# Kernel tuning notes

Hardware: AMD Instinct MI355X
Metric: run time of the kernel (lower is better)

Reference implementation:

```python
import jax, jax.numpy as jnp
import numpy as np

N_NODES = 50000
N_EDGES = 1000000
NEG_SLOPE = 0.2


def _gat_layer(x, W, attn_l, attn_r, bias, src, dst, n_nodes):
    """DGL-style GATConv. x:[N,Fin], W:[H*D,Fin], attn_l/attn_r:[H,D], bias:[H*D].
    Returns [N, H*D] after ReLU activation (flattened heads)."""
    H, D = attn_l.shape
    h = (x @ W.T).reshape(n_nodes, H, D)                    # [N,H,D]
    el = jnp.sum(h * attn_l[None], axis=-1)                 # [N,H]
    er = jnp.sum(h * attn_r[None], axis=-1)                 # [N,H]
    e = jax.nn.leaky_relu(el[src] + er[dst], NEG_SLOPE)     # [E,H]
    # edge softmax over incoming edges per destination node
    emax = jax.ops.segment_max(e, dst, num_segments=n_nodes)  # [N,H]
    emax = jnp.where(jnp.isfinite(emax), emax, 0.0)
    a = jnp.exp(e - emax[dst])                               # [E,H]
    denom = jax.ops.segment_sum(a, dst, num_segments=n_nodes)  # [N,H]
    alpha = a / denom[dst]                                   # [E,H]
    msg = alpha[:, :, None] * h[src]                         # [E,H,D]
    out = jax.ops.segment_sum(msg, dst, num_segments=n_nodes)  # [N,H,D]
    out = out + bias.reshape(1, H, D)
    out = jax.nn.relu(out)
    return out.reshape(n_nodes, H * D)


def setup_inputs() -> dict:
    key = jax.random.key(0)
    ks = jax.random.split(key, 16)
    features = jax.random.normal(ks[0], (N_NODES, 25), dtype=jnp.float32)
    src = jax.random.randint(ks[1], (N_EDGES,), 0, N_NODES, dtype=jnp.int32)
    dst = jax.random.randint(ks[2], (N_EDGES,), 0, N_NODES, dtype=jnp.int32)

    def glorot(k, shape, fan):
        return jax.random.normal(k, shape, dtype=jnp.float32) * (1.0 / np.sqrt(fan))

    # layer 1: in=25, out=10, heads=4
    W1 = glorot(ks[3], (40, 25), 25)
    al1 = glorot(ks[4], (4, 10), 10)
    ar1 = glorot(ks[5], (4, 10), 10)
    b1 = jnp.zeros((40,), dtype=jnp.float32)
    # layer 2: in=40, out=25, heads=4
    W2 = glorot(ks[6], (100, 40), 40)
    al2 = glorot(ks[7], (4, 25), 25)
    ar2 = glorot(ks[8], (4, 25), 25)
    b2 = jnp.zeros((100,), dtype=jnp.float32)
    # layer 3: in=100, out=50, heads=1
    W3 = glorot(ks[9], (50, 100), 100)
    al3 = glorot(ks[10], (1, 50), 50)
    ar3 = glorot(ks[11], (1, 50), 50)
    b3 = jnp.zeros((50,), dtype=jnp.float32)
    # final fc: 50 -> 93
    fc_w = glorot(ks[12], (93, 50), 50)
    fc_b = jnp.zeros((93,), dtype=jnp.float32)
    return {
        "features": features, "src": src, "dst": dst,
        "W1": W1, "al1": al1, "ar1": ar1, "b1": b1,
        "W2": W2, "al2": al2, "ar2": ar2, "b2": b2,
        "W3": W3, "al3": al3, "ar3": ar3, "b3": b3,
        "fc_w": fc_w, "fc_b": fc_b,
    }


def reference(features, src, dst,
              W1, al1, ar1, b1,
              W2, al2, ar2, b2,
              W3, al3, ar3, b3,
              fc_w, fc_b):
    n = features.shape[0]
    h = _gat_layer(features, W1, al1, ar1, b1, src, dst, n)   # [N,40]
    h = _gat_layer(h, W2, al2, ar2, b2, src, dst, n)          # [N,100]
    h = _gat_layer(h, W3, al3, ar3, b3, src, dst, n)          # [N,50]
    return h @ fc_w.T + fc_b                                  # [N,93]
```

## Files before the change

### kernel.cpp

```cpp
#include <hip/hip_runtime.h>
#include <hip/hip_bf16.h>

#ifndef NEG_SLOPE
#define NEG_SLOPE 0.2f
#endif

static inline int cdiv(long long a, long long b) { return (int)((a + b - 1) / b); }

__device__ __forceinline__ float lrelu(float v) { return v > 0.f ? v : NEG_SLOPE * v; }

template <int FIN, int FOUT>
__global__ void k_linear(const float* __restrict__ x, const float* __restrict__ W,
                         float* __restrict__ h, int n_nodes) {
    __shared__ float Ws[FIN * FOUT];
    for (int i = threadIdx.x; i < FIN * FOUT; i += blockDim.x) {
        int f = i / FIN, k = i % FIN;
        Ws[k * FOUT + f] = W[i];
    }
    __syncthreads();
    int idx = blockIdx.x * blockDim.x + threadIdx.x;
    int total = n_nodes * FOUT;
    if (idx >= total) return;
    int n = idx / FOUT, f = idx % FOUT;
    const float* __restrict__ xr = x + (long long)n * FIN;
    float acc = 0.f;
#pragma unroll
    for (int k = 0; k < FIN; ++k) acc += xr[k] * Ws[k * FOUT + f];
    h[idx] = acc;
}

template <int H, int D>
__global__ void k_scores(const float* __restrict__ h, const float* __restrict__ al,
                         const float* __restrict__ ar, float* __restrict__ el,
                         float* __restrict__ er, int n_nodes) {
    int idx = blockIdx.x * blockDim.x + threadIdx.x;
    if (idx >= n_nodes * H) return;
    int n = idx / H, hh = idx % H;
    const float* __restrict__ hr = h + (long long)n * (H * D) + hh * D;
    float sl = 0.f, sr = 0.f;
#pragma unroll
    for (int d0 = 0; d0 < D; ++d0) {
        float v = hr[d0];
        sl += v * al[hh * D + d0];
        sr += v * ar[hh * D + d0];
    }
    el[idx] = sl;
    er[idx] = sr;
}

__global__ void k_deg(const int* __restrict__ dst, int* __restrict__ deg, int n_edges) {
    int e = blockIdx.x * blockDim.x + threadIdx.x;
    if (e >= n_edges) return;
    atomicAdd(&deg[dst[e]], 1);
}

__global__ void k_scan_block(const int* __restrict__ deg, int* __restrict__ incl,
                             int* __restrict__ blocksum, int n) {
    __shared__ int tmp[256];
    int t = threadIdx.x;
    int i = blockIdx.x * 256 + t;
    int v = (i < n) ? deg[i] : 0;
    tmp[t] = v;
    __syncthreads();
    for (int off = 1; off < 256; off <<= 1) {
        int add = (t >= off) ? tmp[t - off] : 0;
        __syncthreads();
        tmp[t] += add;
        __syncthreads();
    }
    if (i < n) incl[i] = tmp[t];
    if (t == 255) blocksum[blockIdx.x] = tmp[t];
}

__global__ void k_scan_top(const int* __restrict__ blocksum, int* __restrict__ blockoff, int nb) {
    __shared__ int tmp[256];
    int t = threadIdx.x;
    int base = 0;
    for (int c = 0; c < nb; c += 256) {
        int i = c + t;
        int v = (i < nb) ? blocksum[i] : 0;
        tmp[t] = v;
        __syncthreads();
        for (int off = 1; off < 256; off <<= 1) {
            int add = (t >= off) ? tmp[t - off] : 0;
            __syncthreads();
            tmp[t] += add;
            __syncthreads();
        }
        if (i < nb) blockoff[i] = base + tmp[t] - v;
        base += tmp[255];
        __syncthreads();
    }
}

__global__ void k_scan_finalize(const int* __restrict__ incl, const int* __restrict__ deg,
                                const int* __restrict__ blockoff, int* __restrict__ rowptr,
                                int n, int n_edges) {
    int i = blockIdx.x * blockDim.x + threadIdx.x;
    if (i < n) rowptr[i] = incl[i] - deg[i] + blockoff[i / 256];
    if (i == 0) rowptr[n] = n_edges;
}

__global__ void k_fill(const int* __restrict__ src, const int* __restrict__ dst,
                       const int* __restrict__ rowptr, int* __restrict__ cursor,
                       int* __restrict__ csr_src, int n_edges) {
    int e = blockIdx.x * blockDim.x + threadIdx.x;
    if (e >= n_edges) return;
    int d = dst[e];
    int pos = atomicAdd(&cursor[d], 1);
    csr_src[rowptr[d] + pos] = src[e];
}

__global__ void k_sort_wave(const int* __restrict__ rowptr, int* __restrict__ csr_src,
                            int n_nodes) {
    int wid = (blockIdx.x * blockDim.x + threadIdx.x) >> 6;
    int lane = threadIdx.x & 63;
    if (wid >= n_nodes) return;
    int s0 = rowptr[wid], e0 = rowptr[wid + 1];
    int d = e0 - s0;
    if (d <= 1) return;
    if (d <= 64) {
        int v = (lane < d) ? csr_src[s0 + lane] : 0x7FFFFFFF;
        int rank = 0;
        for (int k = 0; k < d; ++k) {
            int vk = __shfl(v, k);
            rank += (vk < v || (vk == v && k < lane)) ? 1 : 0;
        }
        if (lane < d) csr_src[s0 + rank] = v;
    } else if (lane == 0) {
        for (int a = s0 + 1; a < e0; ++a) {
            int key = csr_src[a];
            int b = a - 1;
            while (b >= s0 && csr_src[b] > key) { csr_src[b + 1] = csr_src[b]; --b; }
            csr_src[b + 1] = key;
        }
    }
}

template <int FOUT, int H, int D, int EB>
__global__ void k_node_gather(const int* __restrict__ rowptr, const int* __restrict__ csr_src,
                              const float* __restrict__ el, const float* __restrict__ er,
                              const float* __restrict__ h, const float* __restrict__ bias,
                              float* __restrict__ xout, int n_nodes) {
    constexpr int NF = (FOUT + 63) / 64;
    int wid = (blockIdx.x * blockDim.x + threadIdx.x) >> 6;
    int lane = threadIdx.x & 63;
    if (wid >= n_nodes) return;
    int start = rowptr[wid], end = rowptr[wid + 1];

    const int eidx = lane / H;
    const int hh_c = lane % H;
    const float er_c = er[wid * H + hh_c];

    float acc[NF], den[NF];
    int f_i[NF], hh_i[NF];
#pragma unroll
    for (int r = 0; r < NF; ++r) {
        int f = lane + r * 64;
        f_i[r] = f;
        hh_i[r] = (f < FOUT) ? (f / D) : 0;
        acc[r] = 0.f;
        den[r] = 0.f;
    }

    if (start < end) {
        int j0 = start;
        int nb = end - j0;
        if (nb > EB) nb = EB;
        int jj = j0 + (eidx < nb ? eidx : 0);
        int s_c = csr_src[jj];
        float e_c = el[s_c * H + hh_c];

        while (true) {
            int j1 = j0 + nb;
            int nb_n = end - j1;
            if (nb_n > EB) nb_n = EB;
            int s_n = 0;
            float e_n = 0.f;
            if (nb_n > 0) {
                int jj2 = j1 + (eidx < nb_n ? eidx : 0);
                s_n = csr_src[jj2];
                e_n = el[s_n * H + hh_c];
            }
            float p_c = expf(lrelu(e_c + er_c));

            float hv[EB * NF];
#pragma unroll
            for (int e = 0; e < EB; ++e) {
                if (e < nb) {
                    int s = __shfl(s_c, e * H);
                    const float* __restrict__ hrow = h + (long long)s * FOUT;
#pragma unroll
                    for (int r = 0; r < NF; ++r)
                        if (f_i[r] < FOUT) hv[e * NF + r] = hrow[f_i[r]];
                }
            }
#pragma unroll
            for (int e = 0; e < EB; ++e) {
                if (e < nb) {
#pragma unroll
                    for (int r = 0; r < NF; ++r) {
                        float p = __shfl(p_c, e * H + hh_i[r]);
                        if (f_i[r] < FOUT) {
                            den[r] += p;
                            acc[r] += p * hv[e * NF + r];
                        }
                    }
                }
            }
            if (nb_n <= 0) break;
            j0 = j1;
            nb = nb_n;
            s_c = s_n;
            e_c = e_n;
        }
    }

#pragma unroll
    for (int r = 0; r < NF; ++r) {
        if (f_i[r] < FOUT) {
            float val;
            if (end > start) val = acc[r] / den[r] + bias[f_i[r]];
            else val = bias[f_i[r]];
            xout[(long long)wid * FOUT + f_i[r]] = val > 0.f ? val : 0.f;
        }
    }
}

template <int FIN, int FOUT>
__global__ void k_fc(const float* __restrict__ x, const float* __restrict__ W,
                     const float* __restrict__ b, float* __restrict__ out, int n_nodes) {
    __shared__ float Ws[FIN * FOUT];
    for (int i = threadIdx.x; i < FIN * FOUT; i += blockDim.x) {
        int f = i / FIN, k = i % FIN;
        Ws[k * FOUT + f] = W[i];
    }
    __syncthreads();
    int idx = blockIdx.x * blockDim.x + threadIdx.x;
    if (idx >= n_nodes * FOUT) return;
    int n = idx / FOUT, f = idx % FOUT;
    const float* __restrict__ xr = x + (long long)n * FIN;
    float acc = b[f];
#pragma unroll
    for (int k = 0; k < FIN; ++k) acc += xr[k] * Ws[k * FOUT + f];
    out[idx] = acc;
}

template <int FIN, int FOUT, int H, int D, int EB>
static void gat_layer(const float* x, const float* W, const float* al, const float* ar,
                      const float* bias, const int* rowptr, const int* csr_src,
                      int n_nodes, float* bufH, float* el, float* er, float* xnext,
                      hipStream_t stream) {
    int tNF = n_nodes * FOUT;
    k_linear<FIN, FOUT><<<cdiv(tNF, 256), 256, 0, stream>>>(x, W, bufH, n_nodes);
    k_scores<H, D><<<cdiv(n_nodes * H, 256), 256, 0, stream>>>(bufH, al, ar, el, er, n_nodes);
    k_node_gather<FOUT, H, D, EB><<<cdiv((long long)n_nodes * 64, 256), 256, 0, stream>>>(
        rowptr, csr_src, el, er, bufH, bias, xnext, n_nodes);
}

extern "C" void kernel_launch(void* const* d_in, const int* in_sizes, int n_in,
                              void* d_out, int out_size, void* d_ws, size_t ws_size,
                              hipStream_t stream) {
    const float* features = (const float*)d_in[0];
    const int* src = (const int*)d_in[1];
    const int* dst = (const int*)d_in[2];
    const float* W1 = (const float*)d_in[3];
    const float* al1 = (const float*)d_in[4];
    const float* ar1 = (const float*)d_in[5];
    const float* b1 = (const float*)d_in[6];
    const float* W2 = (const float*)d_in[7];
    const float* al2 = (const float*)d_in[8];
    const float* ar2 = (const float*)d_in[9];
    const float* b2 = (const float*)d_in[10];
    const float* W3 = (const float*)d_in[11];
    const float* al3 = (const float*)d_in[12];
    const float* ar3 = (const float*)d_in[13];
    const float* b3 = (const float*)d_in[14];
    const float* fc_w = (const float*)d_in[15];
    const float* fc_b = (const float*)d_in[16];

    const int n_nodes = in_sizes[0] / 25;
    const int n_edges = in_sizes[1];
    const int nblocks_nodes = cdiv(n_nodes, 256);

    char* ws = (char*)d_ws;
    size_t off = 0;
    auto alloc = [&](size_t bytes) {
        char* p = ws + off;
        off += (bytes + 255) & ~(size_t)255;
        return p;
    };
    float* bufA = (float*)alloc((size_t)n_nodes * 100 * sizeof(float));
    float* bufH = (float*)alloc((size_t)n_nodes * 100 * sizeof(float));
    float* el = (float*)alloc((size_t)n_nodes * 4 * sizeof(float));
    float* er = (float*)alloc((size_t)n_nodes * 4 * sizeof(float));
    int* deg = (int*)alloc((size_t)n_nodes * sizeof(int));
    int* incl = (int*)alloc((size_t)n_nodes * sizeof(int));
    int* blocksum = (int*)alloc((size_t)nblocks_nodes * sizeof(int));
    int* blockoff = (int*)alloc((size_t)nblocks_nodes * sizeof(int));
    int* rowptr = (int*)alloc((size_t)(n_nodes + 1) * sizeof(int));
    int* cursor = (int*)alloc((size_t)n_nodes * sizeof(int));
    int* csr_src = (int*)alloc((size_t)n_edges * sizeof(int));
    (void)ws_size;

    hipMemsetAsync(deg, 0, (size_t)n_nodes * sizeof(int), stream);
    hipMemsetAsync(cursor, 0, (size_t)n_nodes * sizeof(int), stream);
    k_deg<<<cdiv(n_edges, 256), 256, 0, stream>>>(dst, deg, n_edges);
    k_scan_block<<<nblocks_nodes, 256, 0, stream>>>(deg, incl, blocksum, n_nodes);
    k_scan_top<<<1, 256, 0, stream>>>(blocksum, blockoff, nblocks_nodes);
    k_scan_finalize<<<cdiv(n_nodes + 1, 256), 256, 0, stream>>>(incl, deg, blockoff, rowptr,
                                                                n_nodes, n_edges);
    k_fill<<<cdiv(n_edges, 256), 256, 0, stream>>>(src, dst, rowptr, cursor, csr_src, n_edges);
    k_sort_wave<<<cdiv((long long)n_nodes * 64, 256), 256, 0, stream>>>(rowptr, csr_src,
                                                                        n_nodes);

    gat_layer<25, 40, 4, 10, 16>(features, W1, al1, ar1, b1, rowptr, csr_src, n_nodes,
                                 bufH, el, er, bufA, stream);
    gat_layer<40, 100, 4, 25, 16>(bufA, W2, al2, ar2, b2, rowptr, csr_src, n_nodes,
                                  bufH, el, er, bufA, stream);
    gat_layer<100, 50, 1, 50, 32>(bufA, W3, al3, ar3, b3, rowptr, csr_src, n_nodes,
                                  bufH, el, er, bufA, stream);

    k_fc<50, 93><<<cdiv((long long)n_nodes * 93, 256), 256, 0, stream>>>(
        bufA, fc_w, fc_b, (float*)d_out, n_nodes);
}
```

Measured before the change: 497.0 us.

## Fold attention vectors into linear weights and vectorize per-node gather with float2

```diff
diff --git a/kernel.cpp b/kernel.cpp
--- a/kernel.cpp
+++ b/kernel.cpp
@@ -9,43 +9,51 @@
 
 __device__ __forceinline__ float lrelu(float v) { return v > 0.f ? v : NEG_SLOPE * v; }
 
-template <int FIN, int FOUT>
-__global__ void k_linear(const float* __restrict__ x, const float* __restrict__ W,
-                         float* __restrict__ h, int n_nodes) {
-    __shared__ float Ws[FIN * FOUT];
-    for (int i = threadIdx.x; i < FIN * FOUT; i += blockDim.x) {
+__global__ void k_build_wext(const float* __restrict__ W1, const float* __restrict__ al1,
+                             const float* __restrict__ ar1, const float* __restrict__ W2,
+                             const float* __restrict__ al2, const float* __restrict__ ar2,
+                             const float* __restrict__ W3, const float* __restrict__ al3,
+                             const float* __restrict__ ar3, float* __restrict__ wx1,
+                             float* __restrict__ wx2, float* __restrict__ wx3) {
+    int b = blockIdx.x;
+    const float *W, *al, *ar;
+    float* wx;
+    int FIN, FOUT, H, D;
+    if (b == 0) { W = W1; al = al1; ar = ar1; wx = wx1; FIN = 25; FOUT = 40; H = 4; D = 10; }
+    else if (b == 1) { W = W2; al = al2; ar = ar2; wx = wx2; FIN = 40; FOUT = 100; H = 4; D = 25; }
+    else { W = W3; al = al3; ar = ar3; wx = wx3; FIN = 100; FOUT = 50; H = 1; D = 50; }
+    for (int i = threadIdx.x; i < FOUT * FIN; i += blockDim.x) wx[i] = W[i];
+    for (int i = threadIdx.x; i < 2 * H * FIN; i += blockDim.x) {
+        int row = i / FIN, k = i % FIN;
+        int h = row % H, isR = row / H;
+        const float* a = isR ? ar : al;
+        float s = 0.f;
+        for (int d = 0; d < D; ++d) s += W[(h * D + d) * FIN + k] * a[h * D + d];
+        wx[(FOUT + isR * H + h) * FIN + k] = s;
+    }
+}
+
+template <int FIN, int FOUT, int H>
+__global__ void k_linear(const float* __restrict__ x, const float* __restrict__ wx,
+                         float* __restrict__ h, float* __restrict__ el, float* __restrict__ er,
+                         int n_nodes) {
+    constexpr int FOUTE = FOUT + 2 * H;
+    __shared__ float Ws[FIN * FOUTE];
+    for (int i = threadIdx.x; i < FIN * FOUTE; i += blockDim.x) {
         int f = i / FIN, k = i % FIN;
-        Ws[k * FOUT + f] = W[i];
+        Ws[k * FOUTE + f] = wx[i];
     }
     __syncthreads();
     int idx = blockIdx.x * blockDim.x + threadIdx.x;
-    int total = n_nodes * FOUT;
-    if (idx >= total) return;
-    int n = idx / FOUT, f = idx % FOUT;
+    if (idx >= n_nodes * FOUTE) return;
+    int n = idx / FOUTE, f = idx % FOUTE;
     const float* __restrict__ xr = x + (long long)n * FIN;
     float acc = 0.f;
 #pragma unroll
-    for (int k = 0; k < FIN; ++k) acc += xr[k] * Ws[k * FOUT + f];
-    h[idx] = acc;
-}
-
-template <int H, int D>
-__global__ void k_scores(const float* __restrict__ h, const float* __restrict__ al,
-                         const float* __restrict__ ar, float* __restrict__ el,
-                         float* __restrict__ er, int n_nodes) {
-    int idx = blockIdx.x * blockDim.x + threadIdx.x;
-    if (idx >= n_nodes * H) return;
-    int n = idx / H, hh = idx % H;
-    const float* __restrict__ hr = h + (long long)n * (H * D) + hh * D;
-    float sl = 0.f, sr = 0.f;
-#pragma unroll
-    for (int d0 = 0; d0 < D; ++d0) {
-        float v = hr[d0];
-        sl += v * al[hh * D + d0];
-        sr += v * ar[hh * D + d0];
-    }
-    el[idx] = sl;
-    er[idx] = sr;
+    for (int k = 0; k < FIN; ++k) acc += xr[k] * Ws[k * FOUTE + f];
+    if (f < FOUT) h[(long long)n * FOUT + f] = acc;
+    else if (f < FOUT + H) el[n * H + (f - FOUT)] = acc;
+    else er[n * H + (f - FOUT - H)] = acc;
 }
 
 __global__ void k_deg(const int* __restrict__ dst, int* __restrict__ deg, int n_edges) {
@@ -138,92 +146,103 @@
 }
 
 template <int FOUT, int H, int D, int EB>
-__global__ void k_node_gather(const int* __restrict__ rowptr, const int* __restrict__ csr_src,
-                              const float* __restrict__ el, const float* __restrict__ er,
-                              const float* __restrict__ h, const float* __restrict__ bias,
-                              float* __restrict__ xout, int n_nodes) {
-    constexpr int NF = (FOUT + 63) / 64;
+__global__ __launch_bounds__(256, 4) void k_node_gather(
+    const int* __restrict__ rowptr, const int* __restrict__ csr_src,
+    const float* __restrict__ el, const float* __restrict__ er, const float* __restrict__ h,
+    const float* __restrict__ bias, float* __restrict__ xout, int n_nodes) {
+    constexpr int P = FOUT / 2;
+    constexpr int NP = (EB * H + 63) / 64;
     int wid = (blockIdx.x * blockDim.x + threadIdx.x) >> 6;
     int lane = threadIdx.x & 63;
     if (wid >= n_nodes) return;
     int start = rowptr[wid], end = rowptr[wid + 1];
 
-    const int eidx = lane / H;
-    const int hh_c = lane % H;
-    const float er_c = er[wid * H + hh_c];
-
-    float acc[NF], den[NF];
-    int f_i[NF], hh_i[NF];
-#pragma unroll
-    for (int r = 0; r < NF; ++r) {
-        int f = lane + r * 64;
-        f_i[r] = f;
-        hh_i[r] = (f < FOUT) ? (f / D) : 0;
-        acc[r] = 0.f;
-        den[r] = 0.f;
-    }
+    const int hh_p = lane % H;
+    const float er_c = er[wid * H + hh_p];
+    const int f0 = 2 * lane, f1 = 2 * lane + 1;
+    const int hh0 = (lane < P) ? f0 / D : 0;
+    const int hh1 = (lane < P) ? f1 / D : 0;
+    float acc0 = 0.f, acc1 = 0.f, den_acc = 0.f;
 
     if (start < end) {
         int j0 = start;
         int nb = end - j0;
         if (nb > EB) nb = EB;
-        int jj = j0 + (eidx < nb ? eidx : 0);
-        int s_c = csr_src[jj];
-        float e_c = el[s_c * H + hh_c];
-
+        int s_c[NP];
+        float e_c[NP];
+#pragma unroll
+        for (int q = 0; q < NP; ++q) {
+            int ei = (q * 64 + lane) / H;
+            s_c[q] = csr_src[j0 + (ei < nb ? ei : 0)];
+            e_c[q] = el[s_c[q] * H + hh_p];
+        }
         while (true) {
             int j1 = j0 + nb;
-            int nb_n = end - j1;
-            if (nb_n > EB) nb_n = EB;
-            int s_n = 0;
-            float e_n = 0.f;
-            if (nb_n > 0) {
-                int jj2 = j1 + (eidx < nb_n ? eidx : 0);
-                s_n = csr_src[jj2];
-                e_n = el[s_n * H + hh_c];
-            }
-            float p_c = expf(lrelu(e_c + er_c));
-
-            float hv[EB * NF];
+            int nbn = end - j1;
+            if (nbn > EB) nbn = EB;
+            int s_n[NP];
+            float e_n[NP];
+            if (nbn > 0) {
+#pragma unroll
+                for (int q = 0; q < NP; ++q) {
+                    int ei = (q * 64 + lane) / H;
+                    s_n[q] = csr_src[j1 + (ei < nbn ? ei : 0)];
+                    e_n[q] = el[s_n[q] * H + hh_p];
+                }
+            }
+            float p_c[NP];
+#pragma unroll
+            for (int q = 0; q < NP; ++q) p_c[q] = expf(lrelu(e_c[q] + er_c));
+            float pd = 0.f;
+#pragma unroll
+            for (int q = 0; q < NP; ++q) {
+                int ei = (q * 64 + lane) / H;
+                pd += (ei < nb) ? p_c[q] : 0.f;
+            }
+#pragma unroll
+            for (int st = H; st < 64; st <<= 1) pd += __shfl_xor(pd, st);
+            den_acc += pd;
+            float2 hv[EB];
 #pragma unroll
             for (int e = 0; e < EB; ++e) {
                 if (e < nb) {
-                    int s = __shfl(s_c, e * H);
-                    const float* __restrict__ hrow = h + (long long)s * FOUT;
-#pragma unroll
-                    for (int r = 0; r < NF; ++r)
-                        if (f_i[r] < FOUT) hv[e * NF + r] = hrow[f_i[r]];
+                    int sreg = __shfl(s_c[(e * H) >> 6], (e * H) & 63);
+                    if (lane < P)
+                        hv[e] = ((const float2*)(h + (long long)sreg * FOUT))[lane];
                 }
             }
 #pragma unroll
             for (int e = 0; e < EB; ++e) {
                 if (e < nb) {
-#pragma unroll
-                    for (int r = 0; r < NF; ++r) {
-                        float p = __shfl(p_c, e * H + hh_i[r]);
-                        if (f_i[r] < FOUT) {
-                            den[r] += p;
-                            acc[r] += p * hv[e * NF + r];
-                        }
+                    float p0 = __shfl(p_c[(e * H) >> 6], ((e * H) & 63) + hh0);
+                    float p1 = __shfl(p_c[(e * H) >> 6], ((e * H) & 63) + hh1);
+                    if (lane < P) {
+                        acc0 += p0 * hv[e].x;
+                        acc1 += p1 * hv[e].y;
                     }
                 }
             }
-            if (nb_n <= 0) break;
+            if (nbn <= 0) break;
             j0 = j1;
-            nb = nb_n;
-            s_c = s_n;
-            e_c = e_n;
-        }
-    }
-
-#pragma unroll
-    for (int r = 0; r < NF; ++r) {
-        if (f_i[r] < FOUT) {
-            float val;
-            if (end > start) val = acc[r] / den[r] + bias[f_i[r]];
-            else val = bias[f_i[r]];
-            xout[(long long)wid * FOUT + f_i[r]] = val > 0.f ? val : 0.f;
-        }
+            nb = nbn;
+#pragma unroll
+            for (int q = 0; q < NP; ++q) {
+                s_c[q] = s_n[q];
+                e_c[q] = e_n[q];
+            }
+        }
+    }
+    if (lane < P) {
+        float d0 = __shfl(den_acc, hh0);
+        float d1 = __shfl(den_acc, hh1);
+        float b0 = bias[f0], b1 = bias[f1];
+        float v0, v1;
+        if (end > start) { v0 = acc0 / d0 + b0; v1 = acc1 / d1 + b1; }
+        else { v0 = b0; v1 = b1; }
+        float2 o;
+        o.x = v0 > 0.f ? v0 : 0.f;
+        o.y = v1 > 0.f ? v1 : 0.f;
+        ((float2*)(xout + (long long)wid * FOUT))[lane] = o;
     }
 }
 
@@ -247,13 +266,12 @@
 }
 
 template <int FIN, int FOUT, int H, int D, int EB>
-static void gat_layer(const float* x, const float* W, const float* al, const float* ar,
-                      const float* bias, const int* rowptr, const int* csr_src,
-                      int n_nodes, float* bufH, float* el, float* er, float* xnext,
-                      hipStream_t stream) {
-    int tNF = n_nodes * FOUT;
-    k_linear<FIN, FOUT><<<cdiv(tNF, 256), 256, 0, stream>>>(x, W, bufH, n_nodes);
-    k_scores<H, D><<<cdiv(n_nodes * H, 256), 256, 0, stream>>>(bufH, al, ar, el, er, n_nodes);
+static void gat_layer(const float* x, const float* wext, const float* bias, const int* rowptr,
+                      const int* csr_src, int n_nodes, float* bufH, float* el, float* er,
+                      float* xnext, hipStream_t stream) {
+    constexpr int FOUTE = FOUT + 2 * H;
+    k_linear<FIN, FOUT, H><<<cdiv((long long)n_nodes * FOUTE, 256), 256, 0, stream>>>(
+        x, wext, bufH, el, er, n_nodes);
     k_node_gather<FOUT, H, D, EB><<<cdiv((long long)n_nodes * 64, 256), 256, 0, stream>>>(
         rowptr, csr_src, el, er, bufH, bias, xnext, n_nodes);
 }
@@ -294,17 +312,22 @@
     float* bufH = (float*)alloc((size_t)n_nodes * 100 * sizeof(float));
     float* el = (float*)alloc((size_t)n_nodes * 4 * sizeof(float));
     float* er = (float*)alloc((size_t)n_nodes * 4 * sizeof(float));
-    int* deg = (int*)alloc((size_t)n_nodes * sizeof(int));
+    int* degcur = (int*)alloc((size_t)2 * n_nodes * sizeof(int));
+    int* deg = degcur;
+    int* cursor = degcur + n_nodes;
     int* incl = (int*)alloc((size_t)n_nodes * sizeof(int));
     int* blocksum = (int*)alloc((size_t)nblocks_nodes * sizeof(int));
     int* blockoff = (int*)alloc((size_t)nblocks_nodes * sizeof(int));
     int* rowptr = (int*)alloc((size_t)(n_nodes + 1) * sizeof(int));
-    int* cursor = (int*)alloc((size_t)n_nodes * sizeof(int));
     int* csr_src = (int*)alloc((size_t)n_edges * sizeof(int));
+    float* wx1 = (float*)alloc((size_t)48 * 25 * sizeof(float));
+    float* wx2 = (float*)alloc((size_t)108 * 40 * sizeof(float));
+    float* wx3 = (float*)alloc((size_t)52 * 100 * sizeof(float));
     (void)ws_size;
 
-    hipMemsetAsync(deg, 0, (size_t)n_nodes * sizeof(int), stream);
-    hipMemsetAsync(cursor, 0, (size_t)n_nodes * sizeof(int), stream);
+    k_build_wext<<<3, 256, 0, stream>>>(W1, al1, ar1, W2, al2, ar2, W3, al3, ar3, wx1, wx2, wx3);
+
+    hipMemsetAsync(degcur, 0, (size_t)2 * n_nodes * sizeof(int), stream);
     k_deg<<<cdiv(n_edges, 256), 256, 0, stream>>>(dst, deg, n_edges);
     k_scan_block<<<nblocks_nodes, 256, 0, stream>>>(deg, incl, blocksum, n_nodes);
     k_scan_top<<<1, 256, 0, stream>>>(blocksum, blockoff, nblocks_nodes);
@@ -314,12 +337,12 @@
     k_sort_wave<<<cdiv((long long)n_nodes * 64, 256), 256, 0, stream>>>(rowptr, csr_src,
                                                                         n_nodes);
 
-    gat_layer<25, 40, 4, 10, 16>(features, W1, al1, ar1, b1, rowptr, csr_src, n_nodes,
-                                 bufH, el, er, bufA, stream);
-    gat_layer<40, 100, 4, 25, 16>(bufA, W2, al2, ar2, b2, rowptr, csr_src, n_nodes,
-                                  bufH, el, er, bufA, stream);
-    gat_layer<100, 50, 1, 50, 32>(bufA, W3, al3, ar3, b3, rowptr, csr_src, n_nodes,
-                                  bufH, el, er, bufA, stream);
+    gat_layer<25, 40, 4, 10, 32>(features, wx1, b1, rowptr, csr_src, n_nodes, bufH, el, er,
+                                 bufA, stream);
+    gat_layer<40, 100, 4, 25, 32>(bufA, wx2, b2, rowptr, csr_src, n_nodes, bufH, el, er,
+                                  bufA, stream);
+    gat_layer<100, 50, 1, 50, 32>(bufA, wx3, b3, rowptr, csr_src, n_nodes, bufH, el, er,
+                                  bufA, stream);
 
     k_fc<50, 93><<<cdiv((long long)n_nodes * 93, 256), 256, 0, stream>>>(
         bufA, fc_w, fc_b, (float*)d_out, n_nodes);
```

Measured after the change: 547.3 us. 10.1% more time.
